# Kernel optimization log

Hardware: AMD Instinct MI355X
Metric: run time of the kernel (lower is better)

Reference implementation:

```python
import jax, jax.numpy as jnp
import numpy as np

N_NODES = 100000
N_EDGES = 1600000
NUM_GRAPHS = 128


def _gcn_layer(x, W, b, senders, receivers, n_node):
    # Linear transform first (cheaper: feature dim small)
    x = x @ W + b  # [N, out]
    ones = jnp.ones(senders.shape[0], dtype=x.dtype)
    deg_s = jax.ops.segment_sum(ones, senders, n_node)     # out-degree
    deg_r = jax.ops.segment_sum(ones, receivers, n_node)   # in-degree
    # symmetric normalization: D^-1/2 A D^-1/2
    x = x * jax.lax.rsqrt(jnp.maximum(deg_s, 1.0))[:, None]
    x = jax.ops.segment_sum(x[senders], receivers, n_node)  # gather-scatter aggregation
    x = x * jax.lax.rsqrt(jnp.maximum(deg_r, 1.0))[:, None]
    return x


def setup_inputs() -> dict:
    key = jax.random.key(0)
    ks = jax.random.split(key, 10)
    x = jax.random.normal(ks[0], (N_NODES, 9), dtype=jnp.float32)
    senders = jax.random.randint(ks[1], (N_EDGES,), 0, N_NODES)
    receivers = jax.random.randint(ks[2], (N_EDGES,), 0, N_NODES)
    batch = jnp.sort(jax.random.randint(ks[3], (N_NODES,), 0, NUM_GRAPHS))
    # learned params (Dense: W [in,out], b [out]) with LeCun-normal-ish scale
    def dense(k, din, dout):
        return jax.random.normal(k, (din, dout), dtype=jnp.float32) / np.sqrt(din)
    W1 = dense(ks[4], 9, 64)
    b1 = jnp.zeros((64,), jnp.float32)
    W2 = dense(ks[5], 64, 128)
    b2 = jnp.zeros((128,), jnp.float32)
    W3 = dense(ks[6], 128, 2)
    b3 = jnp.zeros((2,), jnp.float32)
    return {"x": x, "senders": senders, "receivers": receivers, "batch": batch,
            "num_graphs": NUM_GRAPHS, "W1": W1, "b1": b1, "W2": W2, "b2": b2,
            "W3": W3, "b3": b3}


def reference(x, senders, receivers, batch, num_graphs, W1, b1, W2, b2, W3, b3):
    n_node = x.shape[0]
    x = jax.nn.relu(_gcn_layer(x, W1, b1, senders, receivers, n_node))
    x = jax.nn.relu(_gcn_layer(x, W2, b2, senders, receivers, n_node))
    x = _gcn_layer(x, W3, b3, senders, receivers, n_node)
    # graph-level pooling
    return jax.ops.segment_sum(x, batch, num_graphs)
```

## Files before the change

kernel.cpp:

```cpp
#include <hip/hip_runtime.h>
#include <hip/hip_bf16.h>
#include <cstddef>

#define BCAP 12288
#define BKCHUNK 3200

typedef unsigned short bf16t;
typedef __attribute__((ext_vector_type(8))) short short8;
typedef __attribute__((ext_vector_type(4))) float f32x4;

static __device__ __forceinline__ float bf2f(unsigned h16) {
    return __uint_as_float(h16 << 16);
}
static __device__ __forceinline__ float2 up2(unsigned u) {
    return make_float2(__uint_as_float(u << 16), __uint_as_float(u & 0xffff0000u));
}
static __device__ __forceinline__ bf16t f2bf(float f) {
    unsigned u = __float_as_uint(f);
    u += 0x7fffu + ((u >> 16) & 1u);
    return (bf16t)(u >> 16);
}
static __device__ __forceinline__ unsigned pk2(float a, float b) {
    return (unsigned)f2bf(a) | ((unsigned)f2bf(b) << 16);
}

__global__ void k_bucket(const int* __restrict__ S, const int* __restrict__ R,
                         unsigned* __restrict__ bufR, unsigned short* __restrict__ bufS,
                         int* __restrict__ gCntR, int* __restrict__ gCntS,
                         int nE, int nB) {
    __shared__ int histR[256], lstR[256], baseR[256];
    __shared__ int histS[256], lstS[256], baseS[256];
    __shared__ int sm[256];
    __shared__ unsigned sortedR[BKCHUNK];
    __shared__ unsigned short sortedS[BKCHUNK];
    __shared__ unsigned char bOfR[BKCHUNK], bOfS[BKCHUNK];
    int t = threadIdx.x;
    histR[t] = 0; histS[t] = 0;
    __syncthreads();
    int chunk = (nE + gridDim.x - 1) / gridDim.x;
    int e0 = blockIdx.x * chunk;
    int e1 = min(e0 + chunk, nE);
    for (int e = e0 + t; e < e1; e += blockDim.x) {
        atomicAdd(&histR[R[e] >> 9], 1);
        atomicAdd(&histS[S[e] >> 9], 1);
    }
    __syncthreads();
    int vR = histR[t], vS = histS[t];
    sm[t] = vR;
    __syncthreads();
    for (int off = 1; off < 256; off <<= 1) {
        int y = (t >= off) ? sm[t - off] : 0;
        __syncthreads();
        sm[t] += y;
        __syncthreads();
    }
    lstR[t] = sm[t] - vR;
    __syncthreads();
    sm[t] = vS;
    __syncthreads();
    for (int off = 1; off < 256; off <<= 1) {
        int y = (t >= off) ? sm[t - off] : 0;
        __syncthreads();
        sm[t] += y;
        __syncthreads();
    }
    lstS[t] = sm[t] - vS;
    if (t < nB) {
        baseR[t] = vR ? atomicAdd(&gCntR[t], vR) : 0;
        baseS[t] = vS ? atomicAdd(&gCntS[t], vS) : 0;
    }
    histR[t] = 0; histS[t] = 0;
    __syncthreads();
    for (int e = e0 + t; e < e1; e += blockDim.x) {
        int r = R[e], s = S[e];
        int br = r >> 9;
        int p = lstR[br] + atomicAdd(&histR[br], 1);
        sortedR[p] = ((unsigned)(r & 511) << 23) | (unsigned)s;
        bOfR[p] = (unsigned char)br;
        int bs = s >> 9;
        int p2 = lstS[bs] + atomicAdd(&histS[bs], 1);
        sortedS[p2] = (unsigned short)(s & 511);
        bOfS[p2] = (unsigned char)bs;
    }
    __syncthreads();
    int cnt = e1 - e0;
    for (int i = t; i < cnt; i += blockDim.x) {
        int b = bOfR[i];
        int slot = baseR[b] + (i - lstR[b]);
        if (slot < BCAP) bufR[(size_t)b * BCAP + slot] = sortedR[i];
        int b2 = bOfS[i];
        int slot2 = baseS[b2] + (i - lstS[b2]);
        if (slot2 < BCAP) bufS[(size_t)b2 * BCAP + slot2] = sortedS[i];
    }
}

__global__ void k_pass2(const unsigned* __restrict__ bufR, const unsigned short* __restrict__ bufS,
                        const int* __restrict__ gCntR, const int* __restrict__ gCntS,
                        const float* __restrict__ x,
                        int* __restrict__ csr, int* __restrict__ cur, int* __restrict__ degR,
                        float* __restrict__ inv_r, float* __restrict__ inv_s,
                        bf16t* __restrict__ xs, int nN, int nB) {
    __shared__ int hist[512];
    __shared__ int incl[512];
    __shared__ int curs[512];
    __shared__ int sm[256];
    __shared__ int histS[512];
    int t = threadIdx.x;
    int b = blockIdx.x;
    int v = (t < nB) ? gCntR[t] : 0;
    sm[t] = v;
    __syncthreads();
    for (int off = 1; off < 256; off <<= 1) {
        int y = (t >= off) ? sm[t - off] : 0;
        __syncthreads();
        sm[t] += y;
        __syncthreads();
    }
    int gb = (b == 0) ? 0 : sm[b - 1];
    int cnt = gCntR[b];
    __syncthreads();

    const unsigned* buf = bufR + (size_t)b * BCAP;
    for (int i = t; i < 512; i += blockDim.x) { hist[i] = 0; curs[i] = 0; histS[i] = 0; }
    __syncthreads();
    for (int i = t; i < cnt; i += blockDim.x)
        atomicAdd(&hist[buf[i] >> 23], 1);
    __syncthreads();
    int a0 = hist[2 * t], a1 = hist[2 * t + 1];
    int ps = a0 + a1;
    sm[t] = ps;
    __syncthreads();
    for (int off = 1; off < 256; off <<= 1) {
        int y = (t >= off) ? sm[t - off] : 0;
        __syncthreads();
        sm[t] += y;
        __syncthreads();
    }
    int ex = sm[t] - ps;
    incl[2 * t] = ex + a0;
    incl[2 * t + 1] = ex + a0 + a1;
    __syncthreads();
    int n0 = b << 9;
    for (int i = t; i < 512; i += blockDim.x) {
        int n = n0 + i;
        if (n < nN) {
            int d = hist[i];
            degR[n] = d;
            cur[n] = gb + incl[i];
            inv_r[n] = rsqrtf(fmaxf((float)d, 1.f));
        }
    }
    for (int i = t; i < cnt; i += blockDim.x) {
        unsigned p = buf[i];
        int rl = p >> 23;
        int s = p & 0x7FFFFF;
        int pos = gb + (incl[rl] - hist[rl]) + atomicAdd(&curs[rl], 1);
        csr[pos] = s;
    }
    int cntS = gCntS[b];
    const unsigned short* bufs = bufS + (size_t)b * BCAP;
    for (int i = t; i < cntS; i += blockDim.x)
        atomicAdd(&histS[bufs[i]], 1);
    __syncthreads();
    for (int i = t; i < 512; i += blockDim.x) {
        int n = n0 + i;
        if (n < nN) {
            float is = rsqrtf(fmaxf((float)histS[i], 1.f));
            inv_s[n] = is;
            float w[9];
#pragma unroll
            for (int k = 0; k < 9; k++) w[k] = x[(size_t)n * 9 + k] * is;
            uint4 pa, pb;
            pa.x = pk2(w[0], w[1]); pa.y = pk2(w[2], w[3]);
            pa.z = pk2(w[4], w[5]); pa.w = pk2(w[6], w[7]);
            pb.x = pk2(w[8], is);   pb.y = 0; pb.z = 0; pb.w = 0;
            uint4* o = (uint4*)(xs + (size_t)n * 16);
            o[0] = pa;
            o[1] = pb;
        }
    }
}

__global__ void k_wprep(const float* __restrict__ W2, bf16t* __restrict__ W2f) {
    int tt = blockIdx.x * blockDim.x + threadIdx.x;
    if (tt >= 1024) return;
    int nt = tt >> 7, kh = (tt >> 6) & 1, lane = tt & 63;
    int n = nt * 16 + (lane & 15);
    int k0 = kh * 32 + (lane >> 4) * 8;
    uint4 p;
    p.x = pk2(W2[(k0 + 0) * 128 + n], W2[(k0 + 1) * 128 + n]);
    p.y = pk2(W2[(k0 + 2) * 128 + n], W2[(k0 + 3) * 128 + n]);
    p.z = pk2(W2[(k0 + 4) * 128 + n], W2[(k0 + 5) * 128 + n]);
    p.w = pk2(W2[(k0 + 6) * 128 + n], W2[(k0 + 7) * 128 + n]);
    ((uint4*)W2f)[tt] = p;
}

__global__ void k_h1f(const unsigned* __restrict__ xs32, const float* __restrict__ W1,
                      const float* __restrict__ b1,
                      const int* __restrict__ csr, const int* __restrict__ cur,
                      const int* __restrict__ degR, const float* __restrict__ inv_r,
                      const float* __restrict__ inv_s,
                      bf16t* __restrict__ h1s, float* __restrict__ warr, int nN) {
    __shared__ float Wl[9 * 64];
    __shared__ float bl[64];
    for (int i = threadIdx.x; i < 9 * 64; i += blockDim.x) Wl[i] = W1[i];
    if (threadIdx.x < 64) bl[threadIdx.x] = b1[threadIdx.x];
    __syncthreads();
    int lane = threadIdx.x & 63;
    int wave = threadIdx.x >> 6;
    int n = blockIdx.x * 16 + wave * 4 + (lane >> 4);
    int ql = lane & 15;
    int g = ql >> 2;
    int f2 = ql & 3;
    int nc = min(n, nN - 1);
    int deg = degR[nc];
    int st = cur[nc] - deg;
    float4 A0 = {0.f, 0.f, 0.f, 0.f}, A1 = {0.f, 0.f, 0.f, 0.f};
    int i = 0;
    for (; i + 8 <= deg; i += 8) {
        int ea = csr[st + i + g];
        int eb = csr[st + i + 4 + g];
        uint2 u0 = *(const uint2*)(xs32 + (size_t)ea * 8 + f2 * 2);
        uint2 u1 = *(const uint2*)(xs32 + (size_t)eb * 8 + f2 * 2);
        float2 l0 = up2(u0.x), h0 = up2(u0.y), l1 = up2(u1.x), h1 = up2(u1.y);
        A0.x += l0.x; A0.y += l0.y; A0.z += h0.x; A0.w += h0.y;
        A1.x += l1.x; A1.y += l1.y; A1.z += h1.x; A1.w += h1.y;
    }
    for (; i + 4 <= deg; i += 4) {
        int ea = csr[st + i + g];
        uint2 u0 = *(const uint2*)(xs32 + (size_t)ea * 8 + f2 * 2);
        float2 l0 = up2(u0.x), h0 = up2(u0.y);
        A0.x += l0.x; A0.y += l0.y; A0.z += h0.x; A0.w += h0.y;
    }
    if (g < deg - i) {
        int ea = csr[st + i + g];
        uint2 u0 = *(const uint2*)(xs32 + (size_t)ea * 8 + f2 * 2);
        float2 l0 = up2(u0.x), h0 = up2(u0.y);
        A1.x += l0.x; A1.y += l0.y; A1.z += h0.x; A1.w += h0.y;
    }
    float4 vq = {A0.x + A1.x, A0.y + A1.y, A0.z + A1.z, A0.w + A1.w};
    vq.x += __shfl_xor(vq.x, 4); vq.y += __shfl_xor(vq.y, 4);
    vq.z += __shfl_xor(vq.z, 4); vq.w += __shfl_xor(vq.w, 4);
    vq.x += __shfl_xor(vq.x, 8); vq.y += __shfl_xor(vq.y, 8);
    vq.z += __shfl_xor(vq.z, 8); vq.w += __shfl_xor(vq.w, 8);
    int base = lane & 48;
    float xv[9];
    xv[0] = __shfl(vq.x, base + 0); xv[1] = __shfl(vq.y, base + 0);
    xv[2] = __shfl(vq.z, base + 0); xv[3] = __shfl(vq.w, base + 0);
    xv[4] = __shfl(vq.x, base + 1); xv[5] = __shfl(vq.y, base + 1);
    xv[6] = __shfl(vq.z, base + 1); xv[7] = __shfl(vq.w, base + 1);
    xv[8] = __shfl(vq.x, base + 2);
    float w = __shfl(vq.y, base + 2);
    float ir = inv_r[nc];
    float is = inv_s[nc];
    int c0 = ql * 4;
    float acc[4];
#pragma unroll
    for (int j = 0; j < 4; j++) acc[j] = w * bl[c0 + j];
#pragma unroll
    for (int k = 0; k < 9; k++) {
        float4 wv = *(const float4*)(Wl + k * 64 + c0);
        acc[0] += xv[k] * wv.x;
        acc[1] += xv[k] * wv.y;
        acc[2] += xv[k] * wv.z;
        acc[3] += xv[k] * wv.w;
    }
    if (n < nN) {
        float v0 = fmaxf(acc[0] * ir, 0.f) * is;
        float v1 = fmaxf(acc[1] * ir, 0.f) * is;
        float v2 = fmaxf(acc[2] * ir, 0.f) * is;
        float v3 = fmaxf(acc[3] * ir, 0.f) * is;
        uint2 pv;
        pv.x = pk2(v0, v1);
        pv.y = pk2(v2, v3);
        *(uint2*)(h1s + (size_t)n * 64 + c0) = pv;
        if (ql == 0) warr[n] = w;
    }
}

__global__ void k_agg64h(const unsigned* __restrict__ h32, unsigned* __restrict__ z32,
                         const int* __restrict__ csr, const int* __restrict__ cur,
                         const int* __restrict__ degR, int nN) {
    int lane = threadIdx.x & 63;
    int wave = threadIdx.x >> 6;
    int n = blockIdx.x * 4 + wave;
    int nc = min(n, nN - 1);
    int q = lane >> 4;
    int ql = lane & 15;
    int deg = degR[nc];
    int st = cur[nc] - deg;
    float4 A0 = {0.f, 0.f, 0.f, 0.f}, A1 = A0, A2 = A0, A3 = A0;
    int i = 0;
    for (; i + 16 <= deg; i += 16) {
        int ea = csr[st + i + q];
        int eb = csr[st + i + 4 + q];
        int ec = csr[st + i + 8 + q];
        int ed = csr[st + i + 12 + q];
        uint2 u0 = *(const uint2*)(h32 + (size_t)ea * 32 + ql * 2);
        uint2 u1 = *(const uint2*)(h32 + (size_t)eb * 32 + ql * 2);
        uint2 u2 = *(const uint2*)(h32 + (size_t)ec * 32 + ql * 2);
        uint2 u3 = *(const uint2*)(h32 + (size_t)ed * 32 + ql * 2);
        float2 a = up2(u0.x), b = up2(u0.y);
        A0.x += a.x; A0.y += a.y; A0.z += b.x; A0.w += b.y;
        a = up2(u1.x); b = up2(u1.y);
        A1.x += a.x; A1.y += a.y; A1.z += b.x; A1.w += b.y;
        a = up2(u2.x); b = up2(u2.y);
        A2.x += a.x; A2.y += a.y; A2.z += b.x; A2.w += b.y;
        a = up2(u3.x); b = up2(u3.y);
        A3.x += a.x; A3.y += a.y; A3.z += b.x; A3.w += b.y;
    }
    for (; i + 4 <= deg; i += 4) {
        int ea = csr[st + i + q];
        uint2 u0 = *(const uint2*)(h32 + (size_t)ea * 32 + ql * 2);
        float2 a = up2(u0.x), b = up2(u0.y);
        A0.x += a.x; A0.y += a.y; A0.z += b.x; A0.w += b.y;
    }
    if (q < deg - i) {
        int ea = csr[st + i + q];
        uint2 u0 = *(const uint2*)(h32 + (size_t)ea * 32 + ql * 2);
        float2 a = up2(u0.x), b = up2(u0.y);
        A1.x += a.x; A1.y += a.y; A1.z += b.x; A1.w += b.y;
    }
    float4 v = {(A0.x + A1.x) + (A2.x + A3.x), (A0.y + A1.y) + (A2.y + A3.y),
                (A0.z + A1.z) + (A2.z + A3.z), (A0.w + A1.w) + (A2.w + A3.w)};
    v.x += __shfl_xor(v.x, 16); v.y += __shfl_xor(v.y, 16);
    v.z += __shfl_xor(v.z, 16); v.w += __shfl_xor(v.w, 16);
    v.x += __shfl_xor(v.x, 32); v.y += __shfl_xor(v.y, 32);
    v.z += __shfl_xor(v.z, 32); v.w += __shfl_xor(v.w, 32);
    if (q == 0 && n < nN) {
        uint2 pv;
        pv.x = pk2(v.x, v.y);
        pv.y = pk2(v.z, v.w);
        *(uint2*)(z32 + (size_t)n * 32 + ql * 2) = pv;
    }
}

__global__ void k_lin23m(const unsigned* __restrict__ z32, const bf16t* __restrict__ W2f,
                         const float* __restrict__ b2, const float* __restrict__ W3,
                         const float* __restrict__ inv_r, const float* __restrict__ inv_s,
                         const float* __restrict__ warr, float* __restrict__ t, int nN) {
    __shared__ float b2l[128];
    __shared__ float W3l[256];
    for (int i = threadIdx.x; i < 128; i += blockDim.x) b2l[i] = b2[i];
    for (int i = threadIdx.x; i < 256; i += blockDim.x) W3l[i] = W3[i];
    __syncthreads();
    int lane = threadIdx.x & 63;
    int wave = threadIdx.x >> 6;
    int n0 = blockIdx.x * 64 + wave * 16;
    int m = lane & 15;
    int q = lane >> 4;
    int na = min(n0 + m, nN - 1);
    short8 afr0 = *(const short8*)(z32 + (size_t)na * 32 + q * 4);
    short8 afr1 = *(const short8*)(z32 + (size_t)na * 32 + 16 + q * 4);
    float w4[4], ir4[4], is4[4];
#pragma unroll
    for (int reg = 0; reg < 4; reg++) {
        int nr = min(n0 + q * 4 + reg, nN - 1);
        w4[reg] = warr[nr];
        ir4[reg] = inv_r[nr];
        is4[reg] = inv_s[nr];
    }
    float p0[4] = {0.f, 0.f, 0.f, 0.f}, p1[4] = {0.f, 0.f, 0.f, 0.f};
#pragma unroll
    for (int nt = 0; nt < 8; nt++) {
        short8 b0 = *(const short8*)(W2f + ((size_t)(nt * 2 + 0) * 64 + lane) * 8);
        short8 b1 = *(const short8*)(W2f + ((size_t)(nt * 2 + 1) * 64 + lane) * 8);
        f32x4 acc = {0.f, 0.f, 0.f, 0.f};
        acc = __builtin_amdgcn_mfma_f32_16x16x32_bf16(afr0, b0, acc, 0, 0, 0);
        acc = __builtin_amdgcn_mfma_f32_16x16x32_bf16(afr1, b1, acc, 0, 0, 0);
        int col = nt * 16 + m;
        float bc = b2l[col];
        float w30 = W3l[col * 2 + 0];
        float w31 = W3l[col * 2 + 1];
#pragma unroll
        for (int reg = 0; reg < 4; reg++) {
            float h = fmaxf((acc[reg] + w4[reg] * bc) * ir4[reg], 0.f) * is4[reg];
            p0[reg] += h * w30;
            p1[reg] += h * w31;
        }
    }
#pragma unroll
    for (int mask = 1; mask < 16; mask <<= 1) {
#pragma unroll
        for (int reg = 0; reg < 4; reg++) {
            p0[reg] += __shfl_xor(p0[reg], mask);
            p1[reg] += __shfl_xor(p1[reg], mask);
        }
    }
    if (m == 0) {
#pragma unroll
        for (int reg = 0; reg < 4; reg++) {
            int nr = n0 + q * 4 + reg;
            if (nr < nN) *(float2*)(t + (size_t)nr * 2) = make_float2(p0[reg], p1[reg]);
        }
    }
}

__global__ void k_poolg(const float* __restrict__ t, const float* __restrict__ inv_r,
                        const float* __restrict__ warr, const float* __restrict__ b3,
                        const int* __restrict__ csr, const int* __restrict__ cur,
                        const int* __restrict__ degR, const int* __restrict__ batch,
                        float* out, int nN, int outSize) {
    __shared__ float sm[256];
    for (int i = threadIdx.x; i < 256; i += blockDim.x) sm[i] = 0.f;
    __syncthreads();
    float b30 = b3[0], b31 = b3[1];
    int n = blockIdx.x * blockDim.x + threadIdx.x;
    if (n < nN) {
        int deg = degR[n];
        int st = cur[n] - deg;
        float a0 = 0.f, a1 = 0.f, c0 = 0.f, c1 = 0.f;
        float d0 = 0.f, d1 = 0.f, e0 = 0.f, e1 = 0.f;
        int i = 0;
        for (; i + 4 <= deg; i += 4) {
            int sa = csr[st + i], sb = csr[st + i + 1];
            int sc = csr[st + i + 2], sd = csr[st + i + 3];
            float2 va = ((const float2*)t)[sa];
            float2 vb = ((const float2*)t)[sb];
            float2 vc = ((const float2*)t)[sc];
            float2 vd = ((const float2*)t)[sd];
            a0 += va.x; a1 += va.y;
            c0 += vb.x; c1 += vb.y;
            d0 += vc.x; d1 += vc.y;
            e0 += vd.x; e1 += vd.y;
        }
        for (; i < deg; i++) {
            float2 va = ((const float2*)t)[csr[st + i]];
            a0 += va.x; a1 += va.y;
        }
        float ir = inv_r[n];
        float wb = warr[n] * ir;
        int g = batch[n];
        atomicAdd(&sm[2 * g + 0], ((a0 + c0) + (d0 + e0)) * ir + wb * b30);
        atomicAdd(&sm[2 * g + 1], ((a1 + c1) + (d1 + e1)) * ir + wb * b31);
    }
    __syncthreads();
    for (int i = threadIdx.x; i < outSize; i += blockDim.x) atomicAdd(&out[i], sm[i]);
}

extern "C" void kernel_launch(void* const* d_in, const int* in_sizes, int n_in,
                              void* d_out, int out_size, void* d_ws, size_t ws_size,
                              hipStream_t stream) {
    const float* x     = (const float*)d_in[0];
    const int*   S     = (const int*)d_in[1];
    const int*   R     = (const int*)d_in[2];
    const int*   batch = (const int*)d_in[3];
    const float* W1 = (const float*)d_in[5];
    const float* b1 = (const float*)d_in[6];
    const float* W2 = (const float*)d_in[7];
    const float* b2 = (const float*)d_in[8];
    const float* W3 = (const float*)d_in[9];
    const float* b3 = (const float*)d_in[10];

    int nN = in_sizes[0] / 9;
    int nE = in_sizes[1];
    int nB = (nN + 511) / 512;

    char* ws = (char*)d_ws;
    int*   cur   = (int*)ws;
    int*   degR  = cur + nN;
    float* inv_s = (float*)(degR + nN);
    float* inv_r = inv_s + nN;
    float* warr  = inv_r + nN;
    int*   gCntR = (int*)(warr + nN);
    int*   gCntS = gCntR + 256;
    int*   csr   = gCntS + 256;
    bf16t* xs    = (bf16t*)(csr + nE);
    bf16t* W2f   = xs + (size_t)nN * 16;
    float* regA  = (float*)(W2f + 8192);
    unsigned*       bufR = (unsigned*)regA;
    unsigned short* bufS = (unsigned short*)(bufR + 256 * BCAP);
    bf16t*    h1s = (bf16t*)regA;
    unsigned* z32 = (unsigned*)(h1s + (size_t)nN * 64);
    float*    t   = (float*)(z32 + (size_t)nN * 32);

    const int B = 256;
    int gN = (nN + B - 1) / B;

    hipMemsetAsync(gCntR, 0, 512 * 4, stream);
    k_wprep<<<4, B, 0, stream>>>(W2, W2f);
    k_bucket<<<512, B, 0, stream>>>(S, R, bufR, bufS, gCntR, gCntS, nE, nB);
    k_pass2<<<nB, B, 0, stream>>>(bufR, bufS, gCntR, gCntS, x, csr, cur, degR,
                                  inv_r, inv_s, xs, nN, nB);

    k_h1f<<<(nN + 15) / 16, B, 0, stream>>>((const unsigned*)xs, W1, b1, csr, cur, degR,
                                            inv_r, inv_s, h1s, warr, nN);

    k_agg64h<<<(nN + 3) / 4, B, 0, stream>>>((const unsigned*)h1s, z32, csr, cur, degR, nN);
    k_lin23m<<<(nN + 63) / 64, B, 0, stream>>>(z32, W2f, b2, W3, inv_r, inv_s, warr, t, nN);

    hipMemsetAsync(d_out, 0, (size_t)out_size * 4, stream);
    k_poolg<<<gN, B, 0, stream>>>(t, inv_r, warr, b3, csr, cur, degR, batch,
                                  (float*)d_out, nN, out_size);
}
```

Baseline: 243.3 us.

## Fuse layer-2 aggregation with MFMA linear, shrink buckets, merge weight prep

Several changes land together. The layer-2 gather aggregation is fused into the MFMA linear kernel through a shared-memory tile, which removes the z32 global round trip and one launch. Weight prep is folded into extra blocks of the bucket kernel, the output memset moves into the fused kernel, and buckets shrink to 256 nodes with smaller per-bucket capacity and byte-sized sender buffers. The layer-1 gather loop is also unrolled to four accumulators. The fused kernel has each wave walk 16 nodes one after another, which lowers parallelism and latency hiding. Zeroing dout inside the fused kernel relies on stream ordering ahead of the pooling kernel.

```diff
diff --git a/kernel.cpp b/kernel.cpp
--- a/kernel.cpp
+++ b/kernel.cpp
@@ -2,16 +2,14 @@
 #include <hip/hip_bf16.h>
 #include <cstddef>
 
-#define BCAP 12288
+#define NBMAX 512
+#define BCAP 5120
 #define BKCHUNK 3200
 
 typedef unsigned short bf16t;
 typedef __attribute__((ext_vector_type(8))) short short8;
 typedef __attribute__((ext_vector_type(4))) float f32x4;
 
-static __device__ __forceinline__ float bf2f(unsigned h16) {
-    return __uint_as_float(h16 << 16);
-}
 static __device__ __forceinline__ float2 up2(unsigned u) {
     return make_float2(__uint_as_float(u << 16), __uint_as_float(u & 0xffff0000u));
 }
@@ -25,66 +23,98 @@
 }
 
 __global__ void k_bucket(const int* __restrict__ S, const int* __restrict__ R,
-                         unsigned* __restrict__ bufR, unsigned short* __restrict__ bufS,
+                         unsigned* __restrict__ bufR, unsigned char* __restrict__ bufS,
                          int* __restrict__ gCntR, int* __restrict__ gCntS,
+                         const float* __restrict__ W2, bf16t* __restrict__ W2f,
                          int nE, int nB) {
-    __shared__ int histR[256], lstR[256], baseR[256];
-    __shared__ int histS[256], lstS[256], baseS[256];
+    __shared__ int histR[NBMAX], lstR[NBMAX], baseR[NBMAX];
+    __shared__ int histS[NBMAX], lstS[NBMAX], baseS[NBMAX];
     __shared__ int sm[256];
     __shared__ unsigned sortedR[BKCHUNK];
-    __shared__ unsigned short sortedS[BKCHUNK];
-    __shared__ unsigned char bOfR[BKCHUNK], bOfS[BKCHUNK];
+    __shared__ unsigned short bOfR[BKCHUNK];
+    __shared__ unsigned char sortedS[BKCHUNK];
+    __shared__ unsigned short bOfS[BKCHUNK];
     int t = threadIdx.x;
-    histR[t] = 0; histS[t] = 0;
-    __syncthreads();
-    int chunk = (nE + gridDim.x - 1) / gridDim.x;
+    int nSort = gridDim.x - 4;
+    if (blockIdx.x >= nSort) {
+        int tt = (blockIdx.x - nSort) * blockDim.x + t;
+        if (tt < 1024) {
+            int nt = tt >> 7, kh = (tt >> 6) & 1, lane = tt & 63;
+            int n = nt * 16 + (lane & 15);
+            int k0 = kh * 32 + (lane >> 4) * 8;
+            uint4 p;
+            p.x = pk2(W2[(k0 + 0) * 128 + n], W2[(k0 + 1) * 128 + n]);
+            p.y = pk2(W2[(k0 + 2) * 128 + n], W2[(k0 + 3) * 128 + n]);
+            p.z = pk2(W2[(k0 + 4) * 128 + n], W2[(k0 + 5) * 128 + n]);
+            p.w = pk2(W2[(k0 + 6) * 128 + n], W2[(k0 + 7) * 128 + n]);
+            ((uint4*)W2f)[tt] = p;
+        }
+        return;
+    }
+    for (int i = t; i < NBMAX; i += 256) { histR[i] = 0; histS[i] = 0; }
+    __syncthreads();
+    int chunk = (nE + nSort - 1) / nSort;
     int e0 = blockIdx.x * chunk;
     int e1 = min(e0 + chunk, nE);
-    for (int e = e0 + t; e < e1; e += blockDim.x) {
-        atomicAdd(&histR[R[e] >> 9], 1);
-        atomicAdd(&histS[S[e] >> 9], 1);
-    }
-    __syncthreads();
-    int vR = histR[t], vS = histS[t];
-    sm[t] = vR;
-    __syncthreads();
-    for (int off = 1; off < 256; off <<= 1) {
-        int y = (t >= off) ? sm[t - off] : 0;
+    for (int e = e0 + t; e < e1; e += 256) {
+        atomicAdd(&histR[R[e] >> 8], 1);
+        atomicAdd(&histS[S[e] >> 8], 1);
+    }
+    __syncthreads();
+    {
+        int c0 = histR[2 * t], c1 = histR[2 * t + 1];
+        int ps = c0 + c1;
+        sm[t] = ps;
         __syncthreads();
-        sm[t] += y;
+        for (int off = 1; off < 256; off <<= 1) {
+            int y = (t >= off) ? sm[t - off] : 0;
+            __syncthreads();
+            sm[t] += y;
+            __syncthreads();
+        }
+        int ex = sm[t] - ps;
+        lstR[2 * t] = ex;
+        lstR[2 * t + 1] = ex + c0;
+    }
+    __syncthreads();
+    {
+        int c0 = histS[2 * t], c1 = histS[2 * t + 1];
+        int ps = c0 + c1;
+        sm[t] = ps;
         __syncthreads();
-    }
-    lstR[t] = sm[t] - vR;
-    __syncthreads();
-    sm[t] = vS;
-    __syncthreads();
-    for (int off = 1; off < 256; off <<= 1) {
-        int y = (t >= off) ? sm[t - off] : 0;
-        __syncthreads();
-        sm[t] += y;
-        __syncthreads();
-    }
-    lstS[t] = sm[t] - vS;
-    if (t < nB) {
-        baseR[t] = vR ? atomicAdd(&gCntR[t], vR) : 0;
-        baseS[t] = vS ? atomicAdd(&gCntS[t], vS) : 0;
-    }
-    histR[t] = 0; histS[t] = 0;
-    __syncthreads();
-    for (int e = e0 + t; e < e1; e += blockDim.x) {
+        for (int off = 1; off < 256; off <<= 1) {
+            int y = (t >= off) ? sm[t - off] : 0;
+            __syncthreads();
+            sm[t] += y;
+            __syncthreads();
+        }
+        int ex = sm[t] - ps;
+        lstS[2 * t] = ex;
+        lstS[2 * t + 1] = ex + c0;
+    }
+    __syncthreads();
+    for (int i = t; i < nB; i += 256) {
+        int cR = histR[i];
+        baseR[i] = cR ? atomicAdd(&gCntR[i], cR) : 0;
+        int cS = histS[i];
+        baseS[i] = cS ? atomicAdd(&gCntS[i], cS) : 0;
+    }
+    for (int i = t; i < NBMAX; i += 256) { histR[i] = 0; histS[i] = 0; }
+    __syncthreads();
+    for (int e = e0 + t; e < e1; e += 256) {
         int r = R[e], s = S[e];
-        int br = r >> 9;
+        int br = r >> 8;
         int p = lstR[br] + atomicAdd(&histR[br], 1);
-        sortedR[p] = ((unsigned)(r & 511) << 23) | (unsigned)s;
-        bOfR[p] = (unsigned char)br;
-        int bs = s >> 9;
+        sortedR[p] = ((unsigned)(r & 255) << 24) | (unsigned)s;
+        bOfR[p] = (unsigned short)br;
+        int bs = s >> 8;
         int p2 = lstS[bs] + atomicAdd(&histS[bs], 1);
-        sortedS[p2] = (unsigned short)(s & 511);
-        bOfS[p2] = (unsigned char)bs;
+        sortedS[p2] = (unsigned char)(s & 255);
+        bOfS[p2] = (unsigned short)bs;
     }
     __syncthreads();
     int cnt = e1 - e0;
-    for (int i = t; i < cnt; i += blockDim.x) {
+    for (int i = t; i < cnt; i += 256) {
         int b = bOfR[i];
         int slot = baseR[b] + (i - lstR[b]);
         if (slot < BCAP) bufR[(size_t)b * BCAP + slot] = sortedR[i];
@@ -94,20 +124,41 @@
     }
 }
 
-__global__ void k_pass2(const unsigned* __restrict__ bufR, const unsigned short* __restrict__ bufS,
+__global__ void k_pass2(const unsigned* __restrict__ bufR, const unsigned char* __restrict__ bufS,
                         const int* __restrict__ gCntR, const int* __restrict__ gCntS,
                         const float* __restrict__ x,
                         int* __restrict__ csr, int* __restrict__ cur, int* __restrict__ degR,
                         float* __restrict__ inv_r, float* __restrict__ inv_s,
                         bf16t* __restrict__ xs, int nN, int nB) {
-    __shared__ int hist[512];
-    __shared__ int incl[512];
-    __shared__ int curs[512];
+    __shared__ int hist[256], incl[256], curs[256], histS[256];
     __shared__ int sm[256];
-    __shared__ int histS[512];
+    __shared__ int gex[NBMAX];
     int t = threadIdx.x;
     int b = blockIdx.x;
-    int v = (t < nB) ? gCntR[t] : 0;
+    {
+        int c0 = (2 * t < nB) ? gCntR[2 * t] : 0;
+        int c1 = (2 * t + 1 < nB) ? gCntR[2 * t + 1] : 0;
+        int ps = c0 + c1;
+        sm[t] = ps;
+        __syncthreads();
+        for (int off = 1; off < 256; off <<= 1) {
+            int y = (t >= off) ? sm[t - off] : 0;
+            __syncthreads();
+            sm[t] += y;
+            __syncthreads();
+        }
+        int ex = sm[t] - ps;
+        gex[2 * t] = ex;
+        gex[2 * t + 1] = ex + c0;
+    }
+    hist[t] = 0; curs[t] = 0; histS[t] = 0;
+    __syncthreads();
+    int gb = gex[b];
+    int cnt = gCntR[b];
+    const unsigned* buf = bufR + (size_t)b * BCAP;
+    for (int i = t; i < cnt; i += 256) atomicAdd(&hist[buf[i] >> 24], 1);
+    __syncthreads();
+    int v = hist[t];
     sm[t] = v;
     __syncthreads();
     for (int off = 1; off < 256; off <<= 1) {
@@ -116,83 +167,40 @@
         sm[t] += y;
         __syncthreads();
     }
-    int gb = (b == 0) ? 0 : sm[b - 1];
-    int cnt = gCntR[b];
-    __syncthreads();
-
-    const unsigned* buf = bufR + (size_t)b * BCAP;
-    for (int i = t; i < 512; i += blockDim.x) { hist[i] = 0; curs[i] = 0; histS[i] = 0; }
-    __syncthreads();
-    for (int i = t; i < cnt; i += blockDim.x)
-        atomicAdd(&hist[buf[i] >> 23], 1);
-    __syncthreads();
-    int a0 = hist[2 * t], a1 = hist[2 * t + 1];
-    int ps = a0 + a1;
-    sm[t] = ps;
-    __syncthreads();
-    for (int off = 1; off < 256; off <<= 1) {
-        int y = (t >= off) ? sm[t - off] : 0;
-        __syncthreads();
-        sm[t] += y;
-        __syncthreads();
-    }
-    int ex = sm[t] - ps;
-    incl[2 * t] = ex + a0;
-    incl[2 * t + 1] = ex + a0 + a1;
-    __syncthreads();
-    int n0 = b << 9;
-    for (int i = t; i < 512; i += blockDim.x) {
-        int n = n0 + i;
-        if (n < nN) {
-            int d = hist[i];
-            degR[n] = d;
-            cur[n] = gb + incl[i];
-            inv_r[n] = rsqrtf(fmaxf((float)d, 1.f));
-        }
-    }
-    for (int i = t; i < cnt; i += blockDim.x) {
+    incl[t] = sm[t];
+    __syncthreads();
+    int n0 = b << 8;
+    int n = n0 + t;
+    if (n < nN) {
+        degR[n] = v;
+        cur[n] = gb + incl[t];
+        inv_r[n] = rsqrtf(fmaxf((float)v, 1.f));
+    }
+    for (int i = t; i < cnt; i += 256) {
         unsigned p = buf[i];
-        int rl = p >> 23;
-        int s = p & 0x7FFFFF;
+        int rl = p >> 24;
+        int s = p & 0xFFFFFF;
         int pos = gb + (incl[rl] - hist[rl]) + atomicAdd(&curs[rl], 1);
         csr[pos] = s;
     }
     int cntS = gCntS[b];
-    const unsigned short* bufs = bufS + (size_t)b * BCAP;
-    for (int i = t; i < cntS; i += blockDim.x)
-        atomicAdd(&histS[bufs[i]], 1);
-    __syncthreads();
-    for (int i = t; i < 512; i += blockDim.x) {
-        int n = n0 + i;
-        if (n < nN) {
-            float is = rsqrtf(fmaxf((float)histS[i], 1.f));
-            inv_s[n] = is;
-            float w[9];
-#pragma unroll
-            for (int k = 0; k < 9; k++) w[k] = x[(size_t)n * 9 + k] * is;
-            uint4 pa, pb;
-            pa.x = pk2(w[0], w[1]); pa.y = pk2(w[2], w[3]);
-            pa.z = pk2(w[4], w[5]); pa.w = pk2(w[6], w[7]);
-            pb.x = pk2(w[8], is);   pb.y = 0; pb.z = 0; pb.w = 0;
-            uint4* o = (uint4*)(xs + (size_t)n * 16);
-            o[0] = pa;
-            o[1] = pb;
-        }
-    }
-}
-
-__global__ void k_wprep(const float* __restrict__ W2, bf16t* __restrict__ W2f) {
-    int tt = blockIdx.x * blockDim.x + threadIdx.x;
-    if (tt >= 1024) return;
-    int nt = tt >> 7, kh = (tt >> 6) & 1, lane = tt & 63;
-    int n = nt * 16 + (lane & 15);
-    int k0 = kh * 32 + (lane >> 4) * 8;
-    uint4 p;
-    p.x = pk2(W2[(k0 + 0) * 128 + n], W2[(k0 + 1) * 128 + n]);
-    p.y = pk2(W2[(k0 + 2) * 128 + n], W2[(k0 + 3) * 128 + n]);
-    p.z = pk2(W2[(k0 + 4) * 128 + n], W2[(k0 + 5) * 128 + n]);
-    p.w = pk2(W2[(k0 + 6) * 128 + n], W2[(k0 + 7) * 128 + n]);
-    ((uint4*)W2f)[tt] = p;
+    const unsigned char* bufs = bufS + (size_t)b * BCAP;
+    for (int i = t; i < cntS; i += 256) atomicAdd(&histS[bufs[i]], 1);
+    __syncthreads();
+    if (n < nN) {
+        float is = rsqrtf(fmaxf((float)histS[t], 1.f));
+        inv_s[n] = is;
+        float w[9];
+#pragma unroll
+        for (int k = 0; k < 9; k++) w[k] = x[(size_t)n * 9 + k] * is;
+        uint4 pa, pb;
+        pa.x = pk2(w[0], w[1]); pa.y = pk2(w[2], w[3]);
+        pa.z = pk2(w[4], w[5]); pa.w = pk2(w[6], w[7]);
+        pb.x = pk2(w[8], is);   pb.y = 0; pb.z = 0; pb.w = 0;
+        uint4* o = (uint4*)(xs + (size_t)n * 16);
+        o[0] = pa;
+        o[1] = pb;
+    }
 }
 
 __global__ void k_h1f(const unsigned* __restrict__ xs32, const float* __restrict__ W1,
@@ -215,30 +223,40 @@
     int nc = min(n, nN - 1);
     int deg = degR[nc];
     int st = cur[nc] - deg;
-    float4 A0 = {0.f, 0.f, 0.f, 0.f}, A1 = {0.f, 0.f, 0.f, 0.f};
+    float4 A0 = {0.f, 0.f, 0.f, 0.f}, A1 = A0, A2 = A0, A3 = A0;
     int i = 0;
-    for (; i + 8 <= deg; i += 8) {
+    for (; i + 16 <= deg; i += 16) {
         int ea = csr[st + i + g];
         int eb = csr[st + i + 4 + g];
+        int ec = csr[st + i + 8 + g];
+        int ed = csr[st + i + 12 + g];
         uint2 u0 = *(const uint2*)(xs32 + (size_t)ea * 8 + f2 * 2);
         uint2 u1 = *(const uint2*)(xs32 + (size_t)eb * 8 + f2 * 2);
-        float2 l0 = up2(u0.x), h0 = up2(u0.y), l1 = up2(u1.x), h1 = up2(u1.y);
-        A0.x += l0.x; A0.y += l0.y; A0.z += h0.x; A0.w += h0.y;
-        A1.x += l1.x; A1.y += l1.y; A1.z += h1.x; A1.w += h1.y;
+        uint2 u2 = *(const uint2*)(xs32 + (size_t)ec * 8 + f2 * 2);
+        uint2 u3 = *(const uint2*)(xs32 + (size_t)ed * 8 + f2 * 2);
+        float2 a = up2(u0.x), b = up2(u0.y);
+        A0.x += a.x; A0.y += a.y; A0.z += b.x; A0.w += b.y;
+        a = up2(u1.x); b = up2(u1.y);
+        A1.x += a.x; A1.y += a.y; A1.z += b.x; A1.w += b.y;
+        a = up2(u2.x); b = up2(u2.y);
+        A2.x += a.x; A2.y += a.y; A2.z += b.x; A2.w += b.y;
+        a = up2(u3.x); b = up2(u3.y);
+        A3.x += a.x; A3.y += a.y; A3.z += b.x; A3.w += b.y;
     }
     for (; i + 4 <= deg; i += 4) {
         int ea = csr[st + i + g];
         uint2 u0 = *(const uint2*)(xs32 + (size_t)ea * 8 + f2 * 2);
-        float2 l0 = up2(u0.x), h0 = up2(u0.y);
-        A0.x += l0.x; A0.y += l0.y; A0.z += h0.x; A0.w += h0.y;
+        float2 a = up2(u0.x), b = up2(u0.y);
+        A0.x += a.x; A0.y += a.y; A0.z += b.x; A0.w += b.y;
     }
     if (g < deg - i) {
         int ea = csr[st + i + g];
         uint2 u0 = *(const uint2*)(xs32 + (size_t)ea * 8 + f2 * 2);
-        float2 l0 = up2(u0.x), h0 = up2(u0.y);
-        A1.x += l0.x; A1.y += l0.y; A1.z += h0.x; A1.w += h0.y;
-    }
-    float4 vq = {A0.x + A1.x, A0.y + A1.y, A0.z + A1.z, A0.w + A1.w};
+        float2 a = up2(u0.x), b = up2(u0.y);
+        A1.x += a.x; A1.y += a.y; A1.z += b.x; A1.w += b.y;
+    }
+    float4 vq = {(A0.x + A1.x) + (A2.x + A3.x), (A0.y + A1.y) + (A2.y + A3.y),
+                 (A0.z + A1.z) + (A2.z + A3.z), (A0.w + A1.w) + (A2.w + A3.w)};
     vq.x += __shfl_xor(vq.x, 4); vq.y += __shfl_xor(vq.y, 4);
     vq.z += __shfl_xor(vq.z, 4); vq.w += __shfl_xor(vq.w, 4);
     vq.x += __shfl_xor(vq.x, 8); vq.y += __shfl_xor(vq.y, 8);
@@ -278,84 +296,82 @@
     }
 }
 
-__global__ void k_agg64h(const unsigned* __restrict__ h32, unsigned* __restrict__ z32,
-                         const int* __restrict__ csr, const int* __restrict__ cur,
-                         const int* __restrict__ degR, int nN) {
+__global__ void k_l2f(const unsigned* __restrict__ h32, const bf16t* __restrict__ W2f,
+                      const float* __restrict__ b2, const float* __restrict__ W3,
+                      const float* __restrict__ inv_r, const float* __restrict__ inv_s,
+                      const float* __restrict__ warr,
+                      const int* __restrict__ csr, const int* __restrict__ cur,
+                      const int* __restrict__ degR,
+                      float* __restrict__ t, float* __restrict__ dout, int outSize, int nN) {
+    __shared__ float b2l[128];
+    __shared__ float W3l[256];
+    __shared__ unsigned zl[64 * 36];
+    for (int i = threadIdx.x; i < 128; i += blockDim.x) b2l[i] = b2[i];
+    for (int i = threadIdx.x; i < 256; i += blockDim.x) W3l[i] = W3[i];
+    if (blockIdx.x == 0 && threadIdx.x < outSize) dout[threadIdx.x] = 0.f;
     int lane = threadIdx.x & 63;
     int wave = threadIdx.x >> 6;
-    int n = blockIdx.x * 4 + wave;
-    int nc = min(n, nN - 1);
+    int n0w = blockIdx.x * 64 + wave * 16;
     int q = lane >> 4;
     int ql = lane & 15;
-    int deg = degR[nc];
-    int st = cur[nc] - deg;
-    float4 A0 = {0.f, 0.f, 0.f, 0.f}, A1 = A0, A2 = A0, A3 = A0;
-    int i = 0;
-    for (; i + 16 <= deg; i += 16) {
-        int ea = csr[st + i + q];
-        int eb = csr[st + i + 4 + q];
-        int ec = csr[st + i + 8 + q];
-        int ed = csr[st + i + 12 + q];
-        uint2 u0 = *(const uint2*)(h32 + (size_t)ea * 32 + ql * 2);
-        uint2 u1 = *(const uint2*)(h32 + (size_t)eb * 32 + ql * 2);
-        uint2 u2 = *(const uint2*)(h32 + (size_t)ec * 32 + ql * 2);
-        uint2 u3 = *(const uint2*)(h32 + (size_t)ed * 32 + ql * 2);
-        float2 a = up2(u0.x), b = up2(u0.y);
-        A0.x += a.x; A0.y += a.y; A0.z += b.x; A0.w += b.y;
-        a = up2(u1.x); b = up2(u1.y);
-        A1.x += a.x; A1.y += a.y; A1.z += b.x; A1.w += b.y;
-        a = up2(u2.x); b = up2(u2.y);
-        A2.x += a.x; A2.y += a.y; A2.z += b.x; A2.w += b.y;
-        a = up2(u3.x); b = up2(u3.y);
-        A3.x += a.x; A3.y += a.y; A3.z += b.x; A3.w += b.y;
-    }
-    for (; i + 4 <= deg; i += 4) {
-        int ea = csr[st + i + q];
-        uint2 u0 = *(const uint2*)(h32 + (size_t)ea * 32 + ql * 2);
-        float2 a = up2(u0.x), b = up2(u0.y);
-        A0.x += a.x; A0.y += a.y; A0.z += b.x; A0.w += b.y;
-    }
-    if (q < deg - i) {
-        int ea = csr[st + i + q];
-        uint2 u0 = *(const uint2*)(h32 + (size_t)ea * 32 + ql * 2);
-        float2 a = up2(u0.x), b = up2(u0.y);
-        A1.x += a.x; A1.y += a.y; A1.z += b.x; A1.w += b.y;
-    }
-    float4 v = {(A0.x + A1.x) + (A2.x + A3.x), (A0.y + A1.y) + (A2.y + A3.y),
-                (A0.z + A1.z) + (A2.z + A3.z), (A0.w + A1.w) + (A2.w + A3.w)};
-    v.x += __shfl_xor(v.x, 16); v.y += __shfl_xor(v.y, 16);
-    v.z += __shfl_xor(v.z, 16); v.w += __shfl_xor(v.w, 16);
-    v.x += __shfl_xor(v.x, 32); v.y += __shfl_xor(v.y, 32);
-    v.z += __shfl_xor(v.z, 32); v.w += __shfl_xor(v.w, 32);
-    if (q == 0 && n < nN) {
-        uint2 pv;
-        pv.x = pk2(v.x, v.y);
-        pv.y = pk2(v.z, v.w);
-        *(uint2*)(z32 + (size_t)n * 32 + ql * 2) = pv;
-    }
-}
-
-__global__ void k_lin23m(const unsigned* __restrict__ z32, const bf16t* __restrict__ W2f,
-                         const float* __restrict__ b2, const float* __restrict__ W3,
-                         const float* __restrict__ inv_r, const float* __restrict__ inv_s,
-                         const float* __restrict__ warr, float* __restrict__ t, int nN) {
-    __shared__ float b2l[128];
-    __shared__ float W3l[256];
-    for (int i = threadIdx.x; i < 128; i += blockDim.x) b2l[i] = b2[i];
-    for (int i = threadIdx.x; i < 256; i += blockDim.x) W3l[i] = W3[i];
-    __syncthreads();
-    int lane = threadIdx.x & 63;
-    int wave = threadIdx.x >> 6;
-    int n0 = blockIdx.x * 64 + wave * 16;
-    int m = lane & 15;
-    int q = lane >> 4;
-    int na = min(n0 + m, nN - 1);
-    short8 afr0 = *(const short8*)(z32 + (size_t)na * 32 + q * 4);
-    short8 afr1 = *(const short8*)(z32 + (size_t)na * 32 + 16 + q * 4);
+    for (int j = 0; j < 16; j++) {
+        int nc = min(n0w + j, nN - 1);
+        int deg = degR[nc];
+        int st = cur[nc] - deg;
+        float4 A0 = {0.f, 0.f, 0.f, 0.f}, A1 = A0, A2 = A0, A3 = A0;
+        int i = 0;
+        for (; i + 16 <= deg; i += 16) {
+            int ea = csr[st + i + q];
+            int eb = csr[st + i + 4 + q];
+            int ec = csr[st + i + 8 + q];
+            int ed = csr[st + i + 12 + q];
+            uint2 u0 = *(const uint2*)(h32 + (size_t)ea * 32 + ql * 2);
+            uint2 u1 = *(const uint2*)(h32 + (size_t)eb * 32 + ql * 2);
+            uint2 u2 = *(const uint2*)(h32 + (size_t)ec * 32 + ql * 2);
+            uint2 u3 = *(const uint2*)(h32 + (size_t)ed * 32 + ql * 2);
+            float2 a = up2(u0.x), b = up2(u0.y);
+            A0.x += a.x; A0.y += a.y; A0.z += b.x; A0.w += b.y;
+            a = up2(u1.x); b = up2(u1.y);
+            A1.x += a.x; A1.y += a.y; A1.z += b.x; A1.w += b.y;
+            a = up2(u2.x); b = up2(u2.y);
+            A2.x += a.x; A2.y += a.y; A2.z += b.x; A2.w += b.y;
+            a = up2(u3.x); b = up2(u3.y);
+            A3.x += a.x; A3.y += a.y; A3.z += b.x; A3.w += b.y;
+        }
+        for (; i + 4 <= deg; i += 4) {
+            int ea = csr[st + i + q];
+            uint2 u0 = *(const uint2*)(h32 + (size_t)ea * 32 + ql * 2);
+            float2 a = up2(u0.x), b = up2(u0.y);
+            A0.x += a.x; A0.y += a.y; A0.z += b.x; A0.w += b.y;
+        }
+        if (q < deg - i) {
+            int ea = csr[st + i + q];
+            uint2 u0 = *(const uint2*)(h32 + (size_t)ea * 32 + ql * 2);
+            float2 a = up2(u0.x), b = up2(u0.y);
+            A1.x += a.x; A1.y += a.y; A1.z += b.x; A1.w += b.y;
+        }
+        float4 v = {(A0.x + A1.x) + (A2.x + A3.x), (A0.y + A1.y) + (A2.y + A3.y),
+                    (A0.z + A1.z) + (A2.z + A3.z), (A0.w + A1.w) + (A2.w + A3.w)};
+        v.x += __shfl_xor(v.x, 16); v.y += __shfl_xor(v.y, 16);
+        v.z += __shfl_xor(v.z, 16); v.w += __shfl_xor(v.w, 16);
+        v.x += __shfl_xor(v.x, 32); v.y += __shfl_xor(v.y, 32);
+        v.z += __shfl_xor(v.z, 32); v.w += __shfl_xor(v.w, 32);
+        if (q == 0) {
+            uint2 pv;
+            pv.x = pk2(v.x, v.y);
+            pv.y = pk2(v.z, v.w);
+            *(uint2*)(zl + (wave * 16 + j) * 36 + ql * 2) = pv;
+        }
+    }
+    __syncthreads();
+    int m = ql;
+    int row = wave * 16 + m;
+    short8 afr0 = *(const short8*)(zl + row * 36 + q * 4);
+    short8 afr1 = *(const short8*)(zl + row * 36 + 16 + q * 4);
     float w4[4], ir4[4], is4[4];
 #pragma unroll
     for (int reg = 0; reg < 4; reg++) {
-        int nr = min(n0 + q * 4 + reg, nN - 1);
+        int nr = min(n0w + q * 4 + reg, nN - 1);
         w4[reg] = warr[nr];
         ir4[reg] = inv_r[nr];
         is4[reg] = inv_s[nr];
@@ -390,7 +406,7 @@
     if (m == 0) {
 #pragma unroll
         for (int reg = 0; reg < 4; reg++) {
-            int nr = n0 + q * 4 + reg;
+            int nr = n0w + q * 4 + reg;
             if (nr < nN) *(float2*)(t + (size_t)nr * 2) = make_float2(p0[reg], p1[reg]);
         }
     }
@@ -454,7 +470,7 @@
 
     int nN = in_sizes[0] / 9;
     int nE = in_sizes[1];
-    int nB = (nN + 511) / 512;
+    int nB = (nN + 255) / 256;
 
     char* ws = (char*)d_ws;
     int*   cur   = (int*)ws;
@@ -463,33 +479,30 @@
     float* inv_r = inv_s + nN;
     float* warr  = inv_r + nN;
     int*   gCntR = (int*)(warr + nN);
-    int*   gCntS = gCntR + 256;
-    int*   csr   = gCntS + 256;
+    int*   gCntS = gCntR + NBMAX;
+    int*   csr   = gCntS + NBMAX;
     bf16t* xs    = (bf16t*)(csr + nE);
     bf16t* W2f   = xs + (size_t)nN * 16;
-    float* regA  = (float*)(W2f + 8192);
-    unsigned*       bufR = (unsigned*)regA;
-    unsigned short* bufS = (unsigned short*)(bufR + 256 * BCAP);
-    bf16t*    h1s = (bf16t*)regA;
-    unsigned* z32 = (unsigned*)(h1s + (size_t)nN * 64);
-    float*    t   = (float*)(z32 + (size_t)nN * 32);
+    char*  regA  = (char*)(W2f + 8192);
+    unsigned*      bufR = (unsigned*)regA;
+    unsigned char* bufS = (unsigned char*)(bufR + (size_t)NBMAX * BCAP);
+    bf16t* h1s = (bf16t*)regA;
+    float* t   = (float*)(regA + (size_t)NBMAX * BCAP * 5);
 
     const int B = 256;
-    int gN = (nN + B - 1) / B;
-
-    hipMemsetAsync(gCntR, 0, 512 * 4, stream);
-    k_wprep<<<4, B, 0, stream>>>(W2, W2f);
-    k_bucket<<<512, B, 0, stream>>>(S, R, bufR, bufS, gCntR, gCntS, nE, nB);
+
+    hipMemsetAsync(gCntR, 0, 2 * NBMAX * 4, stream);
+    k_bucket<<<516, B, 0, stream>>>(S, R, bufR, bufS, gCntR, gCntS, W2, W2f, nE, nB);
     k_pass2<<<nB, B, 0, stream>>>(bufR, bufS, gCntR, gCntS, x, csr, cur, degR,
                                   inv_r, inv_s, xs, nN, nB);
 
     k_h1f<<<(nN + 15) / 16, B, 0, stream>>>((const unsigned*)xs, W1, b1, csr, cur, degR,
                                             inv_r, inv_s, h1s, warr, nN);
 
-    k_agg64h<<<(nN + 3) / 4, B, 0, stream>>>((const unsigned*)h1s, z32, csr, cur, degR, nN);
-    k_lin23m<<<(nN + 63) / 64, B, 0, stream>>>(z32, W2f, b2, W3, inv_r, inv_s, warr, t, nN);
-
-    hipMemsetAsync(d_out, 0, (size_t)out_size * 4, stream);
-    k_poolg<<<gN, B, 0, stream>>>(t, inv_r, warr, b3, csr, cur, degR, batch,
-                                  (float*)d_out, nN, out_size);
-}
+    k_l2f<<<(nN + 63) / 64, B, 0, stream>>>((const unsigned*)h1s, W2f, b2, W3,
+                                            inv_r, inv_s, warr, csr, cur, degR,
+                                            t, (float*)d_out, out_size, nN);
+
+    k_poolg<<<(nN + B - 1) / B, B, 0, stream>>>(t, inv_r, warr, b3, csr, cur, degR, batch,
+                                                (float*)d_out, nN, out_size);
+}
```

New measurement: 229.7 us. 1.06x faster.
